# Performance work log

Measured on AMD Instinct MI355X. Metric: run time of the kernel, lower is better.

The kernel has to match this reference:

```python
import jax, jax.numpy as jnp
import numpy as np
import math

EPS = 1e-5
N_HEAD = 16

def act_quant(x):
    # BitNet per-token int8 absmax quant-dequant with straight-through estimator
    scale = 127.0 / jnp.clip(jnp.max(jnp.abs(x), axis=-1, keepdims=True), EPS)
    q = jnp.clip(jnp.round(x * scale), -128.0, 127.0) / scale
    return x + jax.lax.stop_gradient(q - x)

def bit_linear(x, W):
    # BitNet b1.58 ternary weight quant (per-tensor mean-absmax scale), STE
    s = jnp.clip(jnp.mean(jnp.abs(W)), EPS)
    Wq = jnp.clip(jnp.round(W / s), -1.0, 1.0) * s
    Wq = W + jax.lax.stop_gradient(Wq - W)
    return x @ Wq.T

def setup_inputs() -> dict:
    key = jax.random.key(0)
    ks = jax.random.split(key, 5)
    B, T, C = 2, 2048, 2048
    x = jax.random.normal(ks[0], (B, T, C), dtype=jnp.float32)
    std = 1.0 / math.sqrt(C)
    Wq = jax.random.normal(ks[1], (C, C), dtype=jnp.float32) * std
    Wk = jax.random.normal(ks[2], (C, C), dtype=jnp.float32) * std
    Wv = jax.random.normal(ks[3], (C, C), dtype=jnp.float32) * std
    Wp = jax.random.normal(ks[4], (C, C), dtype=jnp.float32) * std
    return {"x": x, "Wq": Wq, "Wk": Wk, "Wv": Wv, "Wp": Wp}

def reference(x, Wq, Wk, Wv, Wp):
    B, T, C = x.shape
    H = N_HEAD
    D = C // H
    xq = act_quant(x)
    # [B, T, C] -> [B, H, T, D]
    def heads(t):
        return t.reshape(B, T, H, D).transpose(0, 2, 1, 3)
    q = act_quant(heads(bit_linear(xq, Wq)))
    k = act_quant(heads(bit_linear(xq, Wk)))
    v = act_quant(heads(bit_linear(xq, Wv)))
    scores = jnp.einsum('bhtd,bhsd->bhts', q, k) * (1.0 / math.sqrt(D))
    w = act_quant(jax.nn.softmax(scores, axis=-1))  # dropout p=0.0 (eval)
    y = act_quant(jnp.einsum('bhts,bhsd->bhtd', w, v))
    y = y.transpose(0, 2, 1, 3).reshape(B, T, C)
    y = act_quant(bit_linear(y, Wp))
    return y
```

## Files before the change

### kernel.cpp

```cpp
#include <hip/hip_runtime.h>
#include <stdint.h>

namespace {

constexpr int B_ = 2, T_ = 2048, C_ = 2048, H_ = 16, D_ = 128;
constexpr int R_ = B_ * T_;
constexpr float EPSF = 1e-5f;
constexpr float INV_SQRT_D = 0.08838834764831845f;
constexpr float LOG2E = 1.4426950408889634f;
constexpr float LOG2_127 = 6.988684686772166f;

constexpr size_t OFF_WSUM = 0;
constexpr size_t OFF_SW   = 64;
constexpr size_t OFF_WT   = 256;
constexpr size_t OFF_XQ   = OFF_WT   + (size_t)4 * C_ * C_;
constexpr size_t OFF_SX   = OFF_XQ   + (size_t)R_ * C_;
constexpr size_t OFF_QKV  = OFF_SX   + (size_t)R_ * 4;
constexpr size_t OFF_SQKV = OFF_QKV  + (size_t)3 * R_ * C_;
constexpr size_t OFF_YQ   = OFF_SQKV + (size_t)3 * R_ * H_ * 4;
constexpr size_t OFF_SY   = OFF_YQ   + (size_t)R_ * C_;
constexpr size_t OFF_OUTP = OFF_SY   + (size_t)R_ * H_ * 4;
constexpr size_t OFF_VT   = OFF_OUTP;

typedef int   i32x4 __attribute__((ext_vector_type(4)));
typedef short s16x8 __attribute__((ext_vector_type(8)));
typedef float f32x4 __attribute__((ext_vector_type(4)));
typedef unsigned int u32x4 __attribute__((ext_vector_type(4)));

__device__ __forceinline__ i32x4 mfma_i8(i32x4 a, i32x4 b, i32x4 c) {
  return __builtin_amdgcn_mfma_i32_16x16x64_i8(a, b, c, 0, 0, 0);
}
__device__ __forceinline__ f32x4 mfma_bf16(s16x8 a, s16x8 b, f32x4 c) {
  return __builtin_amdgcn_mfma_f32_16x16x32_bf16(a, b, c, 0, 0, 0);
}

__device__ __forceinline__ void dma16(const void* g, void* l) {
  __builtin_amdgcn_global_load_lds(
      (const __attribute__((address_space(1))) void*)g,
      (__attribute__((address_space(3))) void*)l, 16, 0, 0);
}

#if __has_builtin(__builtin_amdgcn_exp2f)
__device__ __forceinline__ float fast_exp2(float x) { return __builtin_amdgcn_exp2f(x); }
#else
__device__ __forceinline__ float fast_exp2(float x) { return exp2f(x); }
#endif

__device__ __forceinline__ short f2bf(float f) {
  union { float f; uint32_t u; } v; v.f = f;
  uint32_t r = v.u + 0x7fffu + ((v.u >> 16) & 1u);
  return (short)(r >> 16);
}
__device__ __forceinline__ float bf2f(short h) {
  union { uint32_t u; float f; } v; v.u = ((uint32_t)(uint16_t)h) << 16;
  return v.f;
}

__global__ __launch_bounds__(256) void wabs_sum_kernel(
    const float* __restrict__ W0, const float* __restrict__ W1,
    const float* __restrict__ W2, const float* __restrict__ W3,
    double* __restrict__ wsum)
{
  const int w   = blockIdx.x >> 6;
  const int blk = blockIdx.x & 63;
  const float* W = (w == 0) ? W0 : (w == 1) ? W1 : (w == 2) ? W2 : W3;
  const float4* W4 = (const float4*)W;
  const int n4 = (C_ * C_) / 4;
  double s = 0.0;
  for (int i = blk * 256 + (int)threadIdx.x; i < n4; i += 64 * 256) {
    float4 v = W4[i];
    s += (double)fabsf(v.x) + (double)fabsf(v.y) +
         (double)fabsf(v.z) + (double)fabsf(v.w);
  }
  __shared__ double sm[256];
  sm[threadIdx.x] = s;
  __syncthreads();
  for (int o = 128; o > 0; o >>= 1) {
    if ((int)threadIdx.x < o) sm[threadIdx.x] += sm[threadIdx.x + o];
    __syncthreads();
  }
  if (threadIdx.x == 0) atomicAdd(&wsum[w], sm[0]);
}

__global__ __launch_bounds__(256) void wquant_kernel(
    const float* __restrict__ W0, const float* __restrict__ W1,
    const float* __restrict__ W2, const float* __restrict__ W3,
    const double* __restrict__ wsum, int8_t* __restrict__ Wt, float* __restrict__ sw)
{
  const int w = blockIdx.x >> 10;
  const float* W = (w == 0) ? W0 : (w == 1) ? W1 : (w == 2) ? W2 : W3;
  const int n = C_ * C_;
  const int n4 = n / 4;
  const float s = fmaxf((float)(wsum[w] * (1.0 / (double)n)), EPSF);
  const float4* W4 = (const float4*)W;
  uint32_t* dst4 = (uint32_t*)(Wt + (size_t)w * n);
  const int base = (blockIdx.x & 1023) * 256 + (int)threadIdx.x;
  for (int i = base; i < n4; i += 1024 * 256) {
    float4 v = W4[i];
    union { int8_t b[4]; uint32_t u; } pk;
    pk.b[0] = (int8_t)fminf(fmaxf(rintf(v.x / s), -1.f), 1.f);
    pk.b[1] = (int8_t)fminf(fmaxf(rintf(v.y / s), -1.f), 1.f);
    pk.b[2] = (int8_t)fminf(fmaxf(rintf(v.z / s), -1.f), 1.f);
    pk.b[3] = (int8_t)fminf(fmaxf(rintf(v.w / s), -1.f), 1.f);
    dst4[i] = pk.u;
  }
  if (base == 0) sw[w] = s;
}

__global__ __launch_bounds__(256) void xquant_kernel(
    const float* __restrict__ x, int8_t* __restrict__ xq, float* __restrict__ sx)
{
  const int r = blockIdx.x;
  const float4* xr = (const float4*)(x + (size_t)r * C_);
  float am = 0.f;
  for (int j = threadIdx.x; j < C_ / 4; j += 256) {
    float4 v = xr[j];
    am = fmaxf(am, fmaxf(fmaxf(fabsf(v.x), fabsf(v.y)),
                         fmaxf(fabsf(v.z), fabsf(v.w))));
  }
  __shared__ float sm[256];
  sm[threadIdx.x] = am;
  __syncthreads();
  for (int o = 128; o > 0; o >>= 1) {
    if ((int)threadIdx.x < o) sm[threadIdx.x] = fmaxf(sm[threadIdx.x], sm[threadIdx.x + o]);
    __syncthreads();
  }
  const float m = fmaxf(sm[0], EPSF);
  const float scale = 127.f / m;
  uint32_t* dst4 = (uint32_t*)(xq + (size_t)r * C_);
  for (int j = threadIdx.x; j < C_ / 4; j += 256) {
    float4 v = xr[j];
    union { int8_t b[4]; uint32_t u; } pk;
    pk.b[0] = (int8_t)fminf(fmaxf(rintf(v.x * scale), -128.f), 127.f);
    pk.b[1] = (int8_t)fminf(fmaxf(rintf(v.y * scale), -128.f), 127.f);
    pk.b[2] = (int8_t)fminf(fmaxf(rintf(v.z * scale), -128.f), 127.f);
    pk.b[3] = (int8_t)fminf(fmaxf(rintf(v.w * scale), -128.f), 127.f);
    dst4[j] = pk.u;
  }
  if (threadIdx.x == 0) sx[r] = m / 127.f;
}

__global__ __launch_bounds__(256) void proj_mfma_kernel(
    const int8_t* __restrict__ xq, const float* __restrict__ sx,
    const int8_t* __restrict__ Wt, const float* __restrict__ sw4,
    int8_t* __restrict__ qkv, float* __restrict__ sqkv)
{
  const int h    = blockIdx.x;
  const int r0   = blockIdx.y * 128;
  const int wsel = blockIdx.z;
  const int tid  = (int)threadIdx.x;
  const int wv   = tid >> 6;
  const int lane = tid & 63;
  const int quad = lane >> 4;
  const int l15  = lane & 15;
  const int rh   = wv >> 1, ch = wv & 1;
  const int8_t* Wm = Wt + (size_t)wsel * C_ * C_;

  __shared__ __align__(16) char As[2][8192];
  __shared__ __align__(16) char Bs[2][8192];
  __shared__ int rmaxs[128];
  if (tid < 128) rmaxs[tid] = 0;

  const int s0a   = wv * 128;
  const int rowA0 = (s0a + lane) >> 2;
  const int qdA0  = ((s0a + lane) & 3) ^ (rowA0 & 3);
  const int rowA1 = (s0a + 64 + lane) >> 2;
  const int qdA1  = ((s0a + 64 + lane) & 3) ^ (rowA1 & 3);

  auto stage = [&](int bf, int k0) {
    dma16(xq + (size_t)(r0 + rowA0) * C_ + k0 + qdA0 * 16, &As[bf][(s0a) * 16]);
    dma16(xq + (size_t)(r0 + rowA1) * C_ + k0 + qdA1 * 16, &As[bf][(s0a + 64) * 16]);
    dma16(Wm + (size_t)(h * 128 + rowA0) * C_ + k0 + qdA0 * 16, &Bs[bf][(s0a) * 16]);
    dma16(Wm + (size_t)(h * 128 + rowA1) * C_ + k0 + qdA1 * 16, &Bs[bf][(s0a + 64) * 16]);
  };

  i32x4 acc[4][4];
  #pragma unroll
  for (int i = 0; i < 4; ++i)
    #pragma unroll
    for (int j = 0; j < 4; ++j) acc[i][j] = i32x4{0, 0, 0, 0};

  stage(0, 0);
  for (int kc = 0; kc < 32; ++kc) {
    __syncthreads();
    if (kc + 1 < 32) stage((kc + 1) & 1, (kc + 1) * 64);
    const char* Ab = As[kc & 1];
    const char* Bb = Bs[kc & 1];
    i32x4 a[4], b[4];
    #pragma unroll
    for (int rt = 0; rt < 4; ++rt) {
      const int row = rh * 64 + rt * 16 + l15;
      a[rt] = *(const i32x4*)(Ab + (row * 4 + (quad ^ (row & 3))) * 16);
    }
    #pragma unroll
    for (int ct = 0; ct < 4; ++ct) {
      const int col = ch * 64 + ct * 16 + l15;
      b[ct] = *(const i32x4*)(Bb + (col * 4 + (quad ^ (col & 3))) * 16);
    }
    #pragma unroll
    for (int rt = 0; rt < 4; ++rt)
      #pragma unroll
      for (int ct = 0; ct < 4; ++ct)
        acc[rt][ct] = mfma_i8(a[rt], b[ct], acc[rt][ct]);
  }

  #pragma unroll
  for (int rt = 0; rt < 4; ++rt)
    #pragma unroll
    for (int r = 0; r < 4; ++r) {
      int m = 0;
      #pragma unroll
      for (int ct = 0; ct < 4; ++ct) {
        int v = acc[rt][ct][r];
        int av = v < 0 ? -v : v;
        m = m > av ? m : av;
      }
      #pragma unroll
      for (int mm = 1; mm < 16; mm <<= 1) {
        int o = __shfl_xor(m, mm, 64);
        m = m > o ? m : o;
      }
      if (l15 == 0) atomicMax(&rmaxs[rh * 64 + rt * 16 + quad * 4 + r], m);
    }
  __syncthreads();

  const float swv = sw4[wsel];
  #pragma unroll
  for (int rt = 0; rt < 4; ++rt)
    #pragma unroll
    for (int r = 0; r < 4; ++r) {
      const int rowl = rh * 64 + rt * 16 + quad * 4 + r;
      const int rglob = r0 + rowl;
      const int mN = rmaxs[rowl];
      const float qscale = (mN > 0) ? 127.f / (float)mN : 0.f;
      const int bb = rglob >> 11;
      const int tt = rglob & (T_ - 1);
      const size_t obase = ((size_t)(bb * H_ + h) * T_ + tt) * D_;
      #pragma unroll
      for (int ct = 0; ct < 4; ++ct) {
        const int col = ch * 64 + ct * 16 + l15;
        float q = rintf((float)acc[rt][ct][r] * qscale);
        q = fminf(fmaxf(q, -128.f), 127.f);
        qkv[(size_t)wsel * R_ * C_ + obase + col] = (int8_t)q;
      }
      if (ch == 0 && l15 == 0) {
        float maxq = (float)mN * sx[rglob] * swv;
        sqkv[(size_t)wsel * R_ * H_ + (size_t)(bb * H_ + h) * T_ + tt] =
            fmaxf(maxq, EPSF) / 127.f;
      }
    }
}

__global__ __launch_bounds__(256) void rowmax_kernel(
    const int8_t* __restrict__ qq, const int8_t* __restrict__ kq,
    const float* __restrict__ sk, float* __restrict__ rmax)
{
  const int bh  = blockIdx.x;
  const int q0  = blockIdx.y * 64;
  const int tid = (int)threadIdx.x;
  const int w    = tid >> 6;
  const int lane = tid & 63;
  const int quad = lane >> 4;
  const int l15  = lane & 15;

  i32x4 qf[4][2];
  #pragma unroll
  for (int qt = 0; qt < 4; ++qt)
    #pragma unroll
    for (int hf = 0; hf < 2; ++hf)
      qf[qt][hf] = *(const i32x4*)(qq + ((size_t)bh * T_ + q0 + qt * 16 + l15) * D_ +
                                   hf * 64 + quad * 16);

  const int8_t* kqb = kq + (size_t)bh * T_ * D_ + (size_t)(l15 * D_ + quad * 16);
  const float*  skb = sk + (size_t)bh * T_ + quad * 4;

  float rx[4][4];
  #pragma unroll
  for (int qt = 0; qt < 4; ++qt)
    #pragma unroll
    for (int r = 0; r < 4; ++r) rx[qt][r] = -3e38f;

  const int sbase = w * 512;
  for (int st = 0; st < 8; ++st) {
    const int s0 = sbase + st * 64;
    #pragma unroll
    for (int kt = 0; kt < 4; ++kt) {
      const f32x4 skv = *(const f32x4*)(skb + s0 + kt * 16);
      const i32x4 ka = *(const i32x4*)(kqb + (size_t)(s0 + kt * 16) * D_);
      const i32x4 kb = *(const i32x4*)(kqb + (size_t)(s0 + kt * 16) * D_ + 64);
      #pragma unroll
      for (int qt = 0; qt < 4; ++qt) {
        i32x4 c = i32x4{0, 0, 0, 0};
        c = mfma_i8(ka, qf[qt][0], c);
        c = mfma_i8(kb, qf[qt][1], c);
        #pragma unroll
        for (int r = 0; r < 4; ++r)
          rx[qt][r] = fmaxf(rx[qt][r], (float)c[r] * skv[r]);
      }
    }
  }

  __shared__ float wmx[4][4][16];
  #pragma unroll
  for (int qt = 0; qt < 4; ++qt) {
    float m = fmaxf(fmaxf(rx[qt][0], rx[qt][1]), fmaxf(rx[qt][2], rx[qt][3]));
    m = fmaxf(m, __shfl_xor(m, 16, 64));
    m = fmaxf(m, __shfl_xor(m, 32, 64));
    if (quad == 0) wmx[w][qt][l15] = m;
  }
  __syncthreads();
  if (tid < 64) {
    #pragma unroll
    for (int qt = 0; qt < 4; ++qt) {
      float mm = fmaxf(fmaxf(wmx[0][qt][l15], wmx[1][qt][l15]),
                       fmaxf(wmx[2][qt][l15], wmx[3][qt][l15]));
      if (quad == 0) rmax[(size_t)bh * T_ + q0 + qt * 16 + l15] = mm;
    }
  }
}

__global__ __launch_bounds__(256) void vtrans_kernel(
    const int8_t* __restrict__ vq, const float* __restrict__ sv,
    short* __restrict__ vT)
{
  const int bh = blockIdx.y;
  const int s0 = blockIdx.x * 64;
  const int tid = (int)threadIdx.x;
  __shared__ __align__(16) int8_t Vs[64][144];
  __shared__ float svs[64];
  const int8_t* vbase = vq + ((size_t)bh * T_ + s0) * D_;
  #pragma unroll
  for (int it = 0; it < 2; ++it) {
    int idx = tid + it * 256;
    int row = idx >> 3, seg = idx & 7;
    *(uint4*)(&Vs[row][seg * 16]) = *(const uint4*)(vbase + row * 128 + seg * 16);
  }
  if (tid < 64) svs[tid] = sv[(size_t)bh * T_ + s0 + tid];
  __syncthreads();
  const int d    = tid >> 1;
  const int half = tid & 1;
  const int kh   = half * 32;
  uint32_t oh[16], ol[16];
  #pragma unroll
  for (int i = 0; i < 32; i += 2) {
    const int k0 = kh + i, k1 = kh + i + 1;
    float v0 = (float)(int)Vs[k0][d] * svs[k0];
    float v1 = (float)(int)Vs[k1][d] * svs[k1];
    short h0 = f2bf(v0), h1 = f2bf(v1);
    short l0 = f2bf(v0 - bf2f(h0)), l1 = f2bf(v1 - bf2f(h1));
    oh[i >> 1] = (uint32_t)(uint16_t)h0 | ((uint32_t)(uint16_t)h1 << 16);
    ol[i >> 1] = (uint32_t)(uint16_t)l0 | ((uint32_t)(uint16_t)l1 << 16);
  }
  const int c = (s0 >> 5) + half;
  char* out = (char*)vT + ((((size_t)bh * 128 + d) * 64 + (size_t)c) << 7);
  const int par = d & 7;
  #pragma unroll
  for (int g = 0; g < 4; ++g) {
    uint4 hi, lo;
    hi.x = oh[2 * g];     hi.y = oh[2 * g + 1];
    hi.z = oh[2 * g + 8]; hi.w = oh[2 * g + 9];
    lo.x = ol[2 * g];     lo.y = ol[2 * g + 1];
    lo.z = ol[2 * g + 8]; lo.w = ol[2 * g + 9];
    *(uint4*)(out + (((2 * g + par) & 7) << 4))     = hi;
    *(uint4*)(out + (((2 * g + 1 + par) & 7) << 4)) = lo;
  }
}

__global__ __launch_bounds__(256, 2) void attn_mfma_kernel(
    const int8_t* __restrict__ qq, const int8_t* __restrict__ kq,
    const float* __restrict__ sq, const float* __restrict__ sk,
    const short* __restrict__ vT, const float* __restrict__ rmax,
    int8_t* __restrict__ yq, float* __restrict__ sy)
{
  const int bh  = blockIdx.x;
  const int t0  = blockIdx.y * 128;
  const int tid = (int)threadIdx.x;
  const int w    = tid >> 6;
  const int lane = tid & 63;
  const int quad = lane >> 4;
  const int l15  = lane & 15;

  __shared__ __align__(16) char smem[69632];
  float* sks = (float*)(smem + 61440);

  const int qrow0 = t0 + 32 * w;

  const int8_t* kq_bh = kq + (size_t)bh * T_ * D_;
  const char*   vb    = (const char*)vT + ((size_t)bh << 20);

  const int kslot = w * 64 + lane;
  const int kkey  = kslot >> 3;
  const int ksrc  = ((kslot & 7) ^ (kkey & 7)) * 16;
  auto stageK = [&](int buf, int cc) {
    dma16(kq_bh + (size_t)(cc * 32 + kkey) * 128 + ksrc,
          smem + buf * 4096 + (w * 64) * 16);
  };

  const size_t vlane = (size_t)(w * 32 + (lane >> 3)) * 8192 + (size_t)((lane & 7) * 16);
  auto stageV = [&](int buf, int cc) {
    char* dst = smem + 12288 + buf * 16384 + (w * 32) * 128;
    const char* src = vb + vlane + (size_t)cc * 128;
    #pragma unroll
    for (int j = 0; j < 4; ++j)
      dma16(src + (size_t)(j * 8) * 8192, dst + j * 1024);
  };

  {
    const float* skg = sk + (size_t)bh * T_;
    dma16(skg + (w * 2 + 0) * 256 + lane * 4, smem + 61440 + (w * 2 + 0) * 1024);
    dma16(skg + (w * 2 + 1) * 256 + lane * 4, smem + 61440 + (w * 2 + 1) * 1024);
  }
  stageK(0, 0);
  stageV(0, 0);

  i32x4 qf[2][2];
  #pragma unroll
  for (int qt = 0; qt < 2; ++qt)
    #pragma unroll
    for (int hf = 0; hf < 2; ++hf)
      qf[qt][hf] = *(const i32x4*)(qq + ((size_t)bh * T_ + qrow0 + qt * 16 + l15) * D_ +
                                   hf * 64 + quad * 16);
  float f0[2];
  #pragma unroll
  for (int qt = 0; qt < 2; ++qt)
    f0[qt] = sq[(size_t)bh * T_ + qrow0 + qt * 16 + l15] * INV_SQRT_D;

  __syncthreads();

  float f1[2], g[2];
  #pragma unroll
  for (int qt = 0; qt < 2; ++qt) {
    const float m = rmax[(size_t)bh * T_ + qrow0 + qt * 16 + l15];
    f1[qt] = f0[qt] * LOG2E;
    g[qt]  = LOG2_127 - (m * f0[qt]) * LOG2E;
  }

  float zac[2][4] = {};
  f32x4 yacc[2][8];
  #pragma unroll
  for (int qt = 0; qt < 2; ++qt)
    #pragma unroll
    for (int dt = 0; dt < 8; ++dt) yacc[qt][dt] = f32x4{0.f, 0.f, 0.f, 0.f};

  const int seg_hi = ((2 * quad + l15) & 7) << 4;
  const int seg_lo = ((2 * quad + 1 + l15) & 7) << 4;

  int bc = 0, bn = 1;
  for (int c = 0; c < 64; ++c) {
    const int s0k = c * 32;
    if (c + 1 < 64) {
      stageK(bn, c + 1);
      stageV(bn, c + 1);
      asm volatile("s_waitcnt vmcnt(5)" ::: "memory");
    } else {
      asm volatile("s_waitcnt vmcnt(0)" ::: "memory");
    }
    __builtin_amdgcn_s_barrier();
    asm volatile("" ::: "memory");

    const char* Kb = smem + bc * 4096;
    uint32_t wdw[2][2][2];
    #pragma unroll
    for (int kt = 0; kt < 2; ++kt) {
      const f32x4 skv = *(const f32x4*)(sks + s0k + kt * 16 + quad * 4);
      const int key = kt * 16 + l15;
      const i32x4 ka = *(const i32x4*)(Kb + key * 128 + ((quad ^ (key & 7)) << 4));
      const i32x4 kb = *(const i32x4*)(Kb + key * 128 + (((quad + 4) ^ (key & 7)) << 4));
      #pragma unroll
      for (int qt = 0; qt < 2; ++qt) {
        i32x4 cc = i32x4{0, 0, 0, 0};
        cc = mfma_i8(ka, qf[qt][0], cc);
        cc = mfma_i8(kb, qf[qt][1], cc);
        float wq_[4];
        #pragma unroll
        for (int r = 0; r < 4; ++r) {
          float t = (float)cc[r] * skv[r];
          float wu = fast_exp2(fmaf(t, f1[qt], g[qt]));
          zac[qt][r] += wu;
          wq_[r] = rintf(wu);
        }
        wdw[qt][kt][0] = (__float_as_uint(wq_[0]) >> 16) |
                         (__float_as_uint(wq_[1]) & 0xffff0000u);
        wdw[qt][kt][1] = (__float_as_uint(wq_[2]) >> 16) |
                         (__float_as_uint(wq_[3]) & 0xffff0000u);
      }
    }

    s16x8 wf[2];
    #pragma unroll
    for (int qt = 0; qt < 2; ++qt) {
      u32x4 tw;
      tw[0] = wdw[qt][0][0]; tw[1] = wdw[qt][0][1];
      tw[2] = wdw[qt][1][0]; tw[3] = wdw[qt][1][1];
      wf[qt] = __builtin_bit_cast(s16x8, tw);
    }

    const char* Vc = smem + 12288 + bc * 16384;
    __builtin_amdgcn_s_setprio(1);
    #pragma unroll
    for (int dt = 0; dt < 8; ++dt) {
      const char* rowp = Vc + (dt * 16 + l15) * 128;
      const s16x8 vh = *(const s16x8*)(rowp + seg_hi);
      const s16x8 vl = *(const s16x8*)(rowp + seg_lo);
      yacc[0][dt] = mfma_bf16(wf[0], vh, yacc[0][dt]);
      yacc[0][dt] = mfma_bf16(wf[0], vl, yacc[0][dt]);
      yacc[1][dt] = mfma_bf16(wf[1], vh, yacc[1][dt]);
      yacc[1][dt] = mfma_bf16(wf[1], vl, yacc[1][dt]);
    }
    __builtin_amdgcn_s_setprio(0);

    bc = bn; bn = (bn == 2) ? 0 : bn + 1;
  }

  float zq[2];
  #pragma unroll
  for (int qt = 0; qt < 2; ++qt) {
    float z = (zac[qt][0] + zac[qt][1]) + (zac[qt][2] + zac[qt][3]);
    z += __shfl_xor(z, 16, 64);
    z += __shfl_xor(z, 32, 64);
    zq[qt] = z;
  }

  const int b = bh >> 4;
  const int h = bh & 15;
  #pragma unroll
  for (int qt = 0; qt < 2; ++qt)
    #pragma unroll
    for (int r = 0; r < 4; ++r) {
      const float zr = __shfl(zq[qt], quad * 4 + r, 64);
      float ym = 0.f;
      #pragma unroll
      for (int dt = 0; dt < 8; ++dt) ym = fmaxf(ym, fabsf(yacc[qt][dt][r]));
      #pragma unroll
      for (int mm = 1; mm < 16; mm <<= 1) ym = fmaxf(ym, __shfl_xor(ym, mm, 64));
      const float invz = 1.f / zr;
      const float ymt = fmaxf(ym * invz, EPSF);
      const float fs = 127.f / ymt;
      const int tglob = t0 + 32 * w + qt * 16 + quad * 4 + r;
      const size_t rowbase = ((size_t)(b * T_ + tglob)) * C_ + h * D_;
      #pragma unroll
      for (int dt = 0; dt < 8; ++dt) {
        float yv = yacc[qt][dt][r] * invz;
        float qv = fminf(fmaxf(rintf(yv * fs), -128.f), 127.f);
        yq[rowbase + dt * 16 + l15] = (int8_t)qv;
      }
      if (l15 == 0)
        sy[(size_t)(b * T_ + tglob) * H_ + h] = ymt / 127.f;
    }
}

__global__ __launch_bounds__(256) void outproj_mfma_kernel(
    const int8_t* __restrict__ yq, const float* __restrict__ sy,
    const int8_t* __restrict__ Wt, const float* __restrict__ sw4,
    float* __restrict__ outp)
{
  const int n0  = blockIdx.x * 64;
  const int r0  = blockIdx.y * 128;
  const int tid = (int)threadIdx.x;
  const int wv   = tid >> 6;
  const int lane = tid & 63;
  const int quad = lane >> 4;
  const int l15  = lane & 15;
  const int rh   = wv >> 1, ch = wv & 1;
  const int8_t* Wm = Wt + (size_t)3 * C_ * C_;

  __shared__ __align__(16) char As[2][8192];
  __shared__ __align__(16) char Bs[2][4096];
  __shared__ float sYs[128][16];
  for (int idx = tid; idx < 128 * 16; idx += 256)
    sYs[idx >> 4][idx & 15] = sy[(size_t)(r0 + (idx >> 4)) * H_ + (idx & 15)];

  const int s0a   = wv * 128;
  const int rowA0 = (s0a + lane) >> 2;
  const int qdA0  = ((s0a + lane) & 3) ^ (rowA0 & 3);
  const int rowA1 = (s0a + 64 + lane) >> 2;
  const int qdA1  = ((s0a + 64 + lane) & 3) ^ (rowA1 & 3);
  const int sb    = wv * 64 + lane;
  const int colB  = sb >> 2;
  const int qdB   = (sb & 3) ^ (colB & 3);

  auto stage = [&](int bf, int k0) {
    dma16(yq + (size_t)(r0 + rowA0) * C_ + k0 + qdA0 * 16, &As[bf][(s0a) * 16]);
    dma16(yq + (size_t)(r0 + rowA1) * C_ + k0 + qdA1 * 16, &As[bf][(s0a + 64) * 16]);
    dma16(Wm + (size_t)(n0 + colB) * C_ + k0 + qdB * 16, &Bs[bf][(wv * 64) * 16]);
  };

  i32x4 iacc[4][2];
  f32x4 facc[4][2];
  #pragma unroll
  for (int i = 0; i < 4; ++i)
    #pragma unroll
    for (int j = 0; j < 2; ++j) { iacc[i][j] = i32x4{0,0,0,0}; facc[i][j] = f32x4{0.f,0.f,0.f,0.f}; }

  stage(0, 0);
  for (int kc = 0; kc < 32; ++kc) {
    __syncthreads();
    if (kc + 1 < 32) stage((kc + 1) & 1, (kc + 1) * 64);
    const char* Ab = As[kc & 1];
    const char* Bb = Bs[kc & 1];
    i32x4 a[4], b[2];
    #pragma unroll
    for (int rt = 0; rt < 4; ++rt) {
      const int row = rh * 64 + rt * 16 + l15;
      a[rt] = *(const i32x4*)(Ab + (row * 4 + (quad ^ (row & 3))) * 16);
    }
    #pragma unroll
    for (int ct = 0; ct < 2; ++ct) {
      const int col = ch * 32 + ct * 16 + l15;
      b[ct] = *(const i32x4*)(Bb + (col * 4 + (quad ^ (col & 3))) * 16);
    }
    #pragma unroll
    for (int rt = 0; rt < 4; ++rt)
      #pragma unroll
      for (int ct = 0; ct < 2; ++ct)
        iacc[rt][ct] = mfma_i8(a[rt], b[ct], iacc[rt][ct]);
    if (kc & 1) {
      const int hd = kc >> 1;
      #pragma unroll
      for (int rt = 0; rt < 4; ++rt)
        #pragma unroll
        for (int r = 0; r < 4; ++r) {
          const float s = sYs[rh * 64 + rt * 16 + quad * 4 + r][hd];
          #pragma unroll
          for (int ct = 0; ct < 2; ++ct)
            facc[rt][ct][r] += (float)iacc[rt][ct][r] * s;
        }
      #pragma unroll
      for (int rt = 0; rt < 4; ++rt)
        #pragma unroll
        for (int ct = 0; ct < 2; ++ct) iacc[rt][ct] = i32x4{0,0,0,0};
    }
  }
  const float swp = sw4[3];
  #pragma unroll
  for (int rt = 0; rt < 4; ++rt)
    #pragma unroll
    for (int r = 0; r < 4; ++r) {
      const int rowl = rh * 64 + rt * 16 + quad * 4 + r;
      #pragma unroll
      for (int ct = 0; ct < 2; ++ct)
        outp[(size_t)(r0 + rowl) * C_ + n0 + ch * 32 + ct * 16 + l15] =
            facc[rt][ct][r] * swp;
    }
}

__global__ __launch_bounds__(256) void final_quant_kernel(
    const float* __restrict__ outp, float* __restrict__ out)
{
  const int r = blockIdx.x;
  const float4* xr = (const float4*)(outp + (size_t)r * C_);
  float am = 0.f;
  for (int j = threadIdx.x; j < C_ / 4; j += 256) {
    float4 v = xr[j];
    am = fmaxf(am, fmaxf(fmaxf(fabsf(v.x), fabsf(v.y)),
                         fmaxf(fabsf(v.z), fabsf(v.w))));
  }
  __shared__ float sm[256];
  sm[threadIdx.x] = am;
  __syncthreads();
  for (int o = 128; o > 0; o >>= 1) {
    if ((int)threadIdx.x < o) sm[threadIdx.x] = fmaxf(sm[threadIdx.x], sm[threadIdx.x + o]);
    __syncthreads();
  }
  const float m = fmaxf(sm[0], EPSF);
  const float scale = 127.f / m;
  const float inv = m / 127.f;
  float4* o4 = (float4*)(out + (size_t)r * C_);
  for (int j = threadIdx.x; j < C_ / 4; j += 256) {
    float4 v = xr[j];
    float4 o;
    o.x = fminf(fmaxf(rintf(v.x * scale), -128.f), 127.f) * inv;
    o.y = fminf(fmaxf(rintf(v.y * scale), -128.f), 127.f) * inv;
    o.z = fminf(fmaxf(rintf(v.z * scale), -128.f), 127.f) * inv;
    o.w = fminf(fmaxf(rintf(v.w * scale), -128.f), 127.f) * inv;
    o4[j] = o;
  }
}

}

extern "C" void kernel_launch(void* const* d_in, const int* in_sizes, int n_in,
                              void* d_out, int out_size, void* d_ws, size_t ws_size,
                              hipStream_t stream)
{
  (void)in_sizes; (void)n_in; (void)out_size; (void)ws_size;
  const float* x  = (const float*)d_in[0];
  const float* W0 = (const float*)d_in[1];
  const float* W1 = (const float*)d_in[2];
  const float* W2 = (const float*)d_in[3];
  const float* W3 = (const float*)d_in[4];

  char* ws = (char*)d_ws;
  double* wsum = (double*)(ws + OFF_WSUM);
  float*  swv  = (float*) (ws + OFF_SW);
  int8_t* Wt   = (int8_t*)(ws + OFF_WT);
  int8_t* xq   = (int8_t*)(ws + OFF_XQ);
  float*  sx   = (float*) (ws + OFF_SX);
  int8_t* qkv  = (int8_t*)(ws + OFF_QKV);
  float*  sqkv = (float*) (ws + OFF_SQKV);
  int8_t* yqp  = (int8_t*)(ws + OFF_YQ);
  float*  syp  = (float*) (ws + OFF_SY);
  float*  outp = (float*) (ws + OFF_OUTP);
  short*  vT   = (short*) (ws + OFF_VT);
  float*  rmx  = (float*) (ws + OFF_XQ);

  hipMemsetAsync(d_ws, 0, 256, stream);
  hipLaunchKernelGGL(wabs_sum_kernel, dim3(256), dim3(256), 0, stream, W0, W1, W2, W3, wsum);
  hipLaunchKernelGGL(wquant_kernel, dim3(4096), dim3(256), 0, stream, W0, W1, W2, W3, wsum, Wt, swv);
  hipLaunchKernelGGL(xquant_kernel, dim3(R_), dim3(256), 0, stream, x, xq, sx);
  hipLaunchKernelGGL(proj_mfma_kernel, dim3(H_, R_ / 128, 3), dim3(256), 0, stream,
                     xq, sx, Wt, swv, qkv, sqkv);
  hipLaunchKernelGGL(rowmax_kernel, dim3(B_ * H_, T_ / 64), dim3(256), 0, stream,
                     qkv, qkv + (size_t)R_ * C_, sqkv + (size_t)R_ * H_, rmx);
  hipLaunchKernelGGL(vtrans_kernel, dim3(T_ / 64, B_ * H_), dim3(256), 0, stream,
                     qkv + (size_t)2 * R_ * C_, sqkv + (size_t)2 * R_ * H_, vT);
  hipLaunchKernelGGL(attn_mfma_kernel, dim3(B_ * H_, T_ / 128), dim3(256), 0, stream,
                     qkv, qkv + (size_t)R_ * C_,
                     sqkv, sqkv + (size_t)R_ * H_,
                     vT, rmx, yqp, syp);
  hipLaunchKernelGGL(outproj_mfma_kernel, dim3(C_ / 64, R_ / 128), dim3(256), 0, stream,
                     yqp, syp, Wt, swv, outp);
  hipLaunchKernelGGL(final_quant_kernel, dim3(R_), dim3(256), 0, stream, outp, (float*)d_out);
}
```

Before: 446.4 us.

## Stage K tiles in shared memory with async double buffering in rowmax

The rowmax kernel now gives each wave its own 16 query rows and sweeps all keys, instead of each wave holding 64 queries and covering a quarter of the keys. K tiles and the key scales are loaded into double-buffered shared memory through async DMA, with an XOR swizzle to avoid bank conflicts. This removes the cross-wave max reduction and shares each K load across the four waves, which cuts redundant global traffic. The cost is a block barrier on every 64-key chunk and fewer MFMAs per K fragment read.

```diff
diff --git a/kernel.cpp b/kernel.cpp
--- a/kernel.cpp
+++ b/kernel.cpp
@@ -263,60 +263,62 @@
   const int quad = lane >> 4;
   const int l15  = lane & 15;
 
-  i32x4 qf[4][2];
-  #pragma unroll
-  for (int qt = 0; qt < 4; ++qt)
-    #pragma unroll
-    for (int hf = 0; hf < 2; ++hf)
-      qf[qt][hf] = *(const i32x4*)(qq + ((size_t)bh * T_ + q0 + qt * 16 + l15) * D_ +
-                                   hf * 64 + quad * 16);
-
-  const int8_t* kqb = kq + (size_t)bh * T_ * D_ + (size_t)(l15 * D_ + quad * 16);
-  const float*  skb = sk + (size_t)bh * T_ + quad * 4;
-
-  float rx[4][4];
-  #pragma unroll
-  for (int qt = 0; qt < 4; ++qt)
-    #pragma unroll
-    for (int r = 0; r < 4; ++r) rx[qt][r] = -3e38f;
-
-  const int sbase = w * 512;
-  for (int st = 0; st < 8; ++st) {
-    const int s0 = sbase + st * 64;
+  __shared__ __align__(16) char smem[24576];
+  float* sks = (float*)(smem + 16384);
+
+  const int8_t* kq_bh = kq + (size_t)bh * T_ * D_;
+
+  const int slot0 = w * 128 + lane;
+  const int key0  = slot0 >> 3;
+  const int src0  = ((slot0 & 7) ^ (key0 & 7)) * 16;
+  const int slot1 = w * 128 + 64 + lane;
+  const int key1  = slot1 >> 3;
+  const int src1  = ((slot1 & 7) ^ (key1 & 7)) * 16;
+  auto stageK = [&](int buf, int cc) {
+    dma16(kq_bh + (size_t)(cc * 64 + key0) * 128 + src0, smem + buf * 8192 + w * 2048);
+    dma16(kq_bh + (size_t)(cc * 64 + key1) * 128 + src1, smem + buf * 8192 + w * 2048 + 1024);
+  };
+
+  {
+    const float* skg = sk + (size_t)bh * T_;
+    dma16(skg + (w * 2 + 0) * 256 + lane * 4, smem + 16384 + (w * 2 + 0) * 1024);
+    dma16(skg + (w * 2 + 1) * 256 + lane * 4, smem + 16384 + (w * 2 + 1) * 1024);
+  }
+  stageK(0, 0);
+
+  i32x4 qf[2];
+  #pragma unroll
+  for (int hf = 0; hf < 2; ++hf)
+    qf[hf] = *(const i32x4*)(qq + ((size_t)bh * T_ + q0 + w * 16 + l15) * D_ +
+                             hf * 64 + quad * 16);
+
+  float rx[4];
+  #pragma unroll
+  for (int r = 0; r < 4; ++r) rx[r] = -3e38f;
+
+  for (int cc = 0; cc < 32; ++cc) {
+    __syncthreads();
+    if (cc + 1 < 32) stageK((cc + 1) & 1, cc + 1);
+    const char* Kb = smem + (cc & 1) * 8192;
     #pragma unroll
     for (int kt = 0; kt < 4; ++kt) {
-      const f32x4 skv = *(const f32x4*)(skb + s0 + kt * 16);
-      const i32x4 ka = *(const i32x4*)(kqb + (size_t)(s0 + kt * 16) * D_);
-      const i32x4 kb = *(const i32x4*)(kqb + (size_t)(s0 + kt * 16) * D_ + 64);
-      #pragma unroll
-      for (int qt = 0; qt < 4; ++qt) {
-        i32x4 c = i32x4{0, 0, 0, 0};
-        c = mfma_i8(ka, qf[qt][0], c);
-        c = mfma_i8(kb, qf[qt][1], c);
-        #pragma unroll
-        for (int r = 0; r < 4; ++r)
-          rx[qt][r] = fmaxf(rx[qt][r], (float)c[r] * skv[r]);
-      }
-    }
-  }
-
-  __shared__ float wmx[4][4][16];
-  #pragma unroll
-  for (int qt = 0; qt < 4; ++qt) {
-    float m = fmaxf(fmaxf(rx[qt][0], rx[qt][1]), fmaxf(rx[qt][2], rx[qt][3]));
-    m = fmaxf(m, __shfl_xor(m, 16, 64));
-    m = fmaxf(m, __shfl_xor(m, 32, 64));
-    if (quad == 0) wmx[w][qt][l15] = m;
-  }
-  __syncthreads();
-  if (tid < 64) {
-    #pragma unroll
-    for (int qt = 0; qt < 4; ++qt) {
-      float mm = fmaxf(fmaxf(wmx[0][qt][l15], wmx[1][qt][l15]),
-                       fmaxf(wmx[2][qt][l15], wmx[3][qt][l15]));
-      if (quad == 0) rmax[(size_t)bh * T_ + q0 + qt * 16 + l15] = mm;
-    }
-  }
+      const int key = kt * 16 + l15;
+      const f32x4 skv = *(const f32x4*)(sks + cc * 64 + kt * 16 + quad * 4);
+      const i32x4 ka = *(const i32x4*)(Kb + key * 128 + ((quad ^ (key & 7)) << 4));
+      const i32x4 kb = *(const i32x4*)(Kb + key * 128 + (((quad + 4) ^ (key & 7)) << 4));
+      i32x4 c = i32x4{0, 0, 0, 0};
+      c = mfma_i8(ka, qf[0], c);
+      c = mfma_i8(kb, qf[1], c);
+      #pragma unroll
+      for (int r = 0; r < 4; ++r)
+        rx[r] = fmaxf(rx[r], (float)c[r] * skv[r]);
+    }
+  }
+
+  float m = fmaxf(fmaxf(rx[0], rx[1]), fmaxf(rx[2], rx[3]));
+  m = fmaxf(m, __shfl_xor(m, 16, 64));
+  m = fmaxf(m, __shfl_xor(m, 32, 64));
+  if (quad == 0) rmax[(size_t)bh * T_ + q0 + w * 16 + l15] = m;
 }
 
 __global__ __launch_bounds__(256) void vtrans_kernel(
```

After: 421.0 us. 1.06x faster.
